# Optimization experiments

Hardware: AMD Instinct MI355X
Metric: run time of the kernel (lower is better)

## Reference

```python
import jax, jax.numpy as jnp
import numpy as np

GAMMA = 0.99
EPS = 1e-05
K = 8192   # num_embeddings
D = 256    # embed_dim
B, T = 32, 1024

def setup_inputs() -> dict:
    key = jax.random.key(0)
    k1, k2 = jax.random.split(key)
    ze = jax.random.normal(k1, (B, T, D), dtype=jnp.float32)
    embedW = jax.random.normal(k2, (K, D), dtype=jnp.float32)
    mt = jnp.zeros((K, D), dtype=jnp.float32)
    Nt = jnp.zeros((K,), dtype=jnp.float32)
    return {"ze": ze, "embedW": embedW, "mt": mt, "Nt": Nt}

def reference(ze, embedW, mt, Nt):
    b = ze.shape[0]
    ze_flat = ze.reshape(-1, ze.shape[-1])                      # [N, D]
    # squared euclidean distances: ||z||^2 - 2 z W^T + ||w||^2  -> [N, K]
    dist_mat = (jnp.sum(ze_flat * ze_flat, axis=1, keepdims=True)
                - 2.0 * ze_flat @ embedW.T
                + jnp.sum(embedW * embedW, axis=1)[None, :])
    zq_idx = jnp.argmin(dist_mat, axis=-1)                      # [N]
    zq = embedW[zq_idx]                                         # gather [N, D]
    # EMA codebook update (training mode), one-hot scatter expressed as segment sums
    nt = jax.ops.segment_sum(jnp.ones_like(zq_idx, dtype=jnp.float32), zq_idx, num_segments=K)
    Nt_new = GAMMA * Nt + (1.0 - GAMMA) * nt
    st = jax.ops.segment_sum(ze_flat, zq_idx, num_segments=K)   # one_hot.T @ ze
    mt_new = GAMMA * mt + (1.0 - GAMMA) * st
    n = jnp.sum(Nt_new)
    Nn = (Nt_new + EPS) * n / (n + K * EPS)
    embedW_new = mt_new / Nn[:, None]
    zq = zq.reshape(b, -1, zq.shape[-1])                        # [B, T, D]
    zq_idx = zq_idx.reshape(b, -1)                              # [B, T]
    commit = jnp.mean((jax.lax.stop_gradient(zq) - ze) ** 2)
    zq_st = ze + jax.lax.stop_gradient(zq - ze)                 # straight-through
    return (zq_st, commit, zq_idx, embedW_new, mt_new, Nt_new)
```

## Files before the change

### kernel.cpp

```cpp
#include <hip/hip_runtime.h>
#include <cstddef>
#include <cstdint>

#define GAMMA_F 0.99f
#define OMG_F   0.01f
#define EPS_F   1e-5f
#define KN 8192
#define DD 256
#define NN 32768

#define OFF_ZQ     0
#define OFF_COMMIT 8388608
#define OFF_IDX    8388609
#define OFF_EMB    8421377
#define OFF_MT     10518529
#define OFF_NT     12615681

#define C1 32
#define NCH1 (NN / C1)
#define NREC (NCH1 * 2)
#define C2 32
#define NCH2 (NREC / C2)

typedef _Float16 half8 __attribute__((ext_vector_type(8)));
typedef _Float16 half4 __attribute__((ext_vector_type(4)));
typedef float    f32x4 __attribute__((ext_vector_type(4)));
typedef unsigned long long u64;

__device__ __forceinline__ void gload16(const void* g, void* l) {
    __builtin_amdgcn_global_load_lds(
        (const __attribute__((address_space(1))) unsigned int*)g,
        (__attribute__((address_space(3))) unsigned int*)l, 16, 0, 0);
}

__device__ __forceinline__ u64 packdi(float dist, int n) {
    unsigned u = __float_as_uint(dist);
    u ^= (unsigned)((int)u >> 31) | 0x80000000u;
    return ((u64)u << 32) | (unsigned)n;
}

__global__ __launch_bounds__(256) void conv_hi_kernel(
    const float* __restrict__ x, _Float16* __restrict__ hi) {
    const size_t i0 = ((size_t)blockIdx.x * 256 + threadIdx.x) * 4;
    const float4 v = *(const float4*)(x + i0);
    half4 h;
    h[0] = (_Float16)v.x; h[1] = (_Float16)v.y;
    h[2] = (_Float16)v.z; h[3] = (_Float16)v.w;
    *(half4*)(hi + i0) = h;
}

__global__ __launch_bounds__(64) void convw_wsq_kernel(
    const float* __restrict__ W, _Float16* __restrict__ wh,
    float* __restrict__ wsq) {
    const int k = blockIdx.x;
    const int lane = threadIdx.x;
    const float4 v = *(const float4*)(W + (size_t)k * DD + lane * 4);
    half4 h;
    h[0] = (_Float16)v.x; h[1] = (_Float16)v.y;
    h[2] = (_Float16)v.z; h[3] = (_Float16)v.w;
    *(half4*)(wh + (size_t)k * DD + lane * 4) = h;
    float s = v.x * v.x + v.y * v.y + v.z * v.z + v.w * v.w;
#pragma unroll
    for (int off = 32; off > 0; off >>= 1) s += __shfl_down(s, off, 64);
    if (lane == 0) wsq[k] = s;
}

__global__ __launch_bounds__(256, 4) void screen_kernel(
    const _Float16* __restrict__ zh, const _Float16* __restrict__ wh,
    const float* __restrict__ wsq, u64* __restrict__ tmin2) {
    __shared__ __align__(16) _Float16 As[128 * 64];
    __shared__ __align__(16) _Float16 Bs[128 * 64];
    __shared__ __align__(16) u64 top2[128][2];

    const int tid  = threadIdx.x;
    const int wave = tid >> 6;
    const int lane = tid & 63;
    const int quad = lane >> 4;
    const int col  = lane & 15;
    const int ph = wave & 1;
    const int ch = wave >> 1;
    const int pw = ph * 64;
    const int cw = ch * 64;

    const int bm = blockIdx.x >> 6;
    const int bn = blockIdx.x & 63;
    const int m0 = bm * 128;
    const int n0 = bn * 128;

    f32x4 acc[4][4];
#pragma unroll
    for (int i = 0; i < 4; i++)
#pragma unroll
        for (int j = 0; j < 4; j++) acc[i][j] = (f32x4){0.f, 0.f, 0.f, 0.f};

    for (int c = 0; c < 4; ++c) {
        const int d0 = c * 64;
        __syncthreads();
#pragma unroll
        for (int i = 0; i < 4; ++i) {
            const int clin = (wave * 4 + i) * 64 + lane;
            const int mrow = clin >> 3;
            const int p = clin & 7;
            const int q = p ^ (mrow & 7);
            gload16(zh + (size_t)(m0 + mrow) * DD + d0 + q * 8,
                    As + (wave * 4 + i) * 512);
            gload16(wh + (size_t)(n0 + mrow) * DD + d0 + q * 8,
                    Bs + (wave * 4 + i) * 512);
        }
        __syncthreads();

#pragma unroll
        for (int kk = 0; kk < 2; ++kk) {
            half8 a[4], b[4];
#pragma unroll
            for (int t = 0; t < 4; ++t) {
                const int cr = cw + t * 16 + col;
                const int pr = pw + t * 16 + col;
                const int cc = kk * 4 + quad;
                a[t] = *(const half8*)(Bs + cr * 64 + (cc ^ (cr & 7)) * 8);
                b[t] = *(const half8*)(As + pr * 64 + (cc ^ (pr & 7)) * 8);
            }
#pragma unroll
            for (int ci = 0; ci < 4; ++ci)
#pragma unroll
                for (int pj = 0; pj < 4; ++pj)
                    acc[ci][pj] = __builtin_amdgcn_mfma_f32_16x16x32_f16(
                        a[ci], b[pj], acc[ci][pj], 0, 0, 0);
        }
    }

    float wq[4][4];
#pragma unroll
    for (int ci = 0; ci < 4; ++ci) {
        const float4 t = *(const float4*)(wsq + n0 + cw + ci * 16 + quad * 4);
        wq[ci][0] = t.x + 4096.f; wq[ci][1] = t.y + 4096.f;
        wq[ci][2] = t.z + 4096.f; wq[ci][3] = t.w + 4096.f;
    }
    const unsigned base7 = (unsigned)(cw + quad * 4);

#pragma unroll
    for (int pj = 0; pj < 4; ++pj) {
        unsigned t0 = 0xFFFFFFFFu, t1 = 0xFFFFFFFFu;
#pragma unroll
        for (int ci = 0; ci < 4; ++ci)
#pragma unroll
            for (int v = 0; v < 4; ++v) {
                const float dist = fmaf(-2.0f, acc[ci][pj][v], wq[ci][v]);
                const unsigned x = (__float_as_uint(dist) & ~127u) |
                                   (base7 + ci * 16 + v);
                const unsigned mx = t0 > x ? t0 : x;
                t0 = t0 < x ? t0 : x;
                t1 = t1 < mx ? t1 : mx;
            }
#pragma unroll
        for (int mk = 16; mk < 64; mk <<= 1) {
            const unsigned o0 = __shfl_xor(t0, mk, 64);
            const unsigned o1 = __shfl_xor(t1, mk, 64);
            const unsigned lo = t0 < o0 ? t0 : o0;
            const unsigned hi = t0 < o0 ? o0 : t0;
            const unsigned mn = t1 < o1 ? t1 : o1;
            t0 = lo;
            t1 = hi < mn ? hi : mn;
        }
        if (quad == 0)
            top2[pw + pj * 16 + col][ch] = ((u64)t1 << 32) | t0;
    }
    __syncthreads();
    if (tid < 128) {
        const u64 e0 = top2[tid][0], e1 = top2[tid][1];
        const unsigned a0 = (unsigned)e0, a1 = (unsigned)(e0 >> 32);
        const unsigned b0 = (unsigned)e1, b1 = (unsigned)(e1 >> 32);
        const unsigned t0 = a0 < b0 ? a0 : b0;
        const unsigned hi = a0 < b0 ? b0 : a0;
        const unsigned mn = a1 < b1 ? a1 : b1;
        const unsigned t1 = hi < mn ? hi : mn;
        const unsigned c1 = n0 + (t0 & 127u);
        const unsigned c2 = n0 + (t1 & 127u);
        const u64 ent = (u64)(t0 & ~127u) | ((u64)c1 << 32) | ((u64)c2 << 48);
        tmin2[(size_t)bn * NN + m0 + tid] = ent;
    }
}

__global__ __launch_bounds__(256) void compact_kernel(
    const u64* __restrict__ tmin2,
    unsigned* __restrict__ cnt, unsigned* __restrict__ slots,
    unsigned* __restrict__ hist_zero,
    const float* __restrict__ mt_in, float* __restrict__ mt_out) {
    const int tid = threadIdx.x;
    const int gid = blockIdx.x * 256 + tid;
    if (gid < KN) hist_zero[gid] = 0u;
    if (gid < KN * DD / 4) {
        const float4 m = *(const float4*)(mt_in + (size_t)gid * 4);
        float4 r;
        r.x = GAMMA_F * m.x; r.y = GAMMA_F * m.y;
        r.z = GAMMA_F * m.z; r.w = GAMMA_F * m.w;
        *(float4*)(mt_out + (size_t)gid * 4) = r;
    }

    const int lane = tid & 63;
    const int n = blockIdx.x * 4 + (tid >> 6);
    const u64 e = tmin2[(size_t)lane * NN + n];
    const float d1 = __uint_as_float((unsigned)e);
    float mn = d1;
#pragma unroll
    for (int off = 32; off > 0; off >>= 1)
        mn = fminf(mn, __shfl_xor(mn, off, 64));
    const bool q = d1 <= mn + 1.0f;
    const u64 bal = __ballot(q);
    if (q) {
        const int rank = __popcll(bal & ((1ull << lane) - 1ull));
        if (rank < 16) {
            slots[(size_t)n * 32 + 2 * rank + 0] = (unsigned)(e >> 32) & 0xffffu;
            slots[(size_t)n * 32 + 2 * rank + 1] = (unsigned)(e >> 48);
        }
    }
    if (lane == 0) {
        unsigned c = 2u * (unsigned)__popcll(bal);
        cnt[n] = c < 32u ? c : 32u;
    }
}

__global__ __launch_bounds__(256) void rescore_gather_kernel(
    const float* __restrict__ ze, const float* __restrict__ W,
    const unsigned* __restrict__ cnt, const unsigned* __restrict__ slots,
    float* __restrict__ idxf, float* __restrict__ zq_out,
    unsigned* __restrict__ hist, float* __restrict__ partials) {
    const int tid = threadIdx.x;
    const int lane = tid & 63;
    const int n = blockIdx.x * 4 + (tid >> 6);
    const float4 z = *(const float4*)(ze + (size_t)n * DD + lane * 4);
    const unsigned m = cnt[n];
    u64 best = ~0ull;
    for (unsigned j = 0; j < m; ++j) {
        const unsigned c = slots[(size_t)n * 32 + j];
        const float4 w = *(const float4*)(W + (size_t)c * DD + lane * 4);
        float dot = z.x * w.x + z.y * w.y + z.z * w.z + z.w * w.w;
        float wq  = w.x * w.x + w.y * w.y + w.z * w.z + w.w * w.w;
#pragma unroll
        for (int off = 32; off > 0; off >>= 1) {
            dot += __shfl_xor(dot, off, 64);
            wq  += __shfl_xor(wq, off, 64);
        }
        const float dist = fmaf(-2.0f, dot, wq);
        const u64 pk = packdi(dist, (int)c);
        best = best < pk ? best : pk;
    }
    const int idx = (int)(unsigned)(best & 0xFFFFFFFFull);
    if (lane == 0) {
        idxf[n] = (float)idx;
        atomicAdd(hist + idx, 1u);
    }

    const float4 w = *(const float4*)(W + (size_t)idx * DD + lane * 4);
    float4 d, o;
    d.x = w.x - z.x; d.y = w.y - z.y; d.z = w.z - z.z; d.w = w.w - z.w;
    o.x = z.x + d.x; o.y = z.y + d.y; o.z = z.z + d.z; o.w = z.w + d.w;
    *(float4*)(zq_out + (size_t)n * DD + lane * 4) = o;

    float c = d.x * d.x + d.y * d.y + d.z * d.z + d.w * d.w;
#pragma unroll
    for (int off = 32; off > 0; off >>= 1) c += __shfl_down(c, off, 64);

    __shared__ float wsum[4];
    if (lane == 0) wsum[tid >> 6] = c;
    __syncthreads();
    if (tid == 0)
        partials[blockIdx.x] = wsum[0] + wsum[1] + wsum[2] + wsum[3];
}

__global__ __launch_bounds__(256) void prefix_kernel(
    const float* __restrict__ Nt_in, float* __restrict__ ntn,
    const float* __restrict__ partials, float* __restrict__ commit_out,
    unsigned* __restrict__ offsets) {
    const int t = threadIdx.x;
    unsigned* hist = (unsigned*)ntn;
    const int base = t * 32;
    unsigned loc[32];
    unsigned sum = 0;
#pragma unroll
    for (int i = 0; i < 32; ++i) { loc[i] = hist[base + i]; sum += loc[i]; }

    __shared__ unsigned ssum[256];
    __shared__ float cred[256];
    ssum[t] = sum;
    float cp = 0.f;
    for (int i = t; i < NN / 4; i += 256) cp += partials[i];
    cred[t] = cp;
    __syncthreads();

    for (int off = 1; off < 256; off <<= 1) {
        const unsigned v = (t >= off) ? ssum[t - off] : 0u;
        __syncthreads();
        ssum[t] += v;
        __syncthreads();
    }
    unsigned run = (t > 0) ? ssum[t - 1] : 0u;

    for (int off = 128; off > 0; off >>= 1) {
        if (t < off) cred[t] += cred[t + off];
        __syncthreads();
    }
    if (t == 0) *commit_out = cred[0] * (1.0f / 8388608.0f);

#pragma unroll
    for (int i = 0; i < 32; ++i) {
        offsets[base + i] = run;
        run += loc[i];
    }
#pragma unroll
    for (int i = 0; i < 32; ++i)
        ntn[base + i] = GAMMA_F * Nt_in[base + i] + OMG_F * (float)loc[i];
}

__global__ __launch_bounds__(256) void scatter_kernel(
    const float* __restrict__ idxf, unsigned* __restrict__ offsets,
    unsigned* __restrict__ perm, unsigned* __restrict__ codes) {
    const int n = blockIdx.x * 256 + threadIdx.x;
    const int idx = (int)idxf[n];
    const unsigned pos = atomicAdd(offsets + idx, 1u);
    perm[pos] = n;
    codes[pos] = (unsigned)idx;
}

__global__ __launch_bounds__(256) void mt1_kernel(
    const float* __restrict__ ze, const float* __restrict__ mt_in,
    const unsigned* __restrict__ perm, const unsigned* __restrict__ codes,
    float* __restrict__ mt_out, unsigned* __restrict__ prec,
    float* __restrict__ pdata) {
    const int tid = threadIdx.x;
    const int lane = tid & 63;
    const int w = blockIdx.x * 4 + (tid >> 6);
    const int j0 = w * C1;

    unsigned ccur = codes[j0];
    bool first = true;
    float4 acc = {0.f, 0.f, 0.f, 0.f};

    for (int j = j0; j < j0 + C1; ++j) {
        const unsigned c = codes[j];
        if (c != ccur) {
            if (first) {
                *(float4*)(pdata + (size_t)(2 * w) * DD + lane * 4) = acc;
                if (lane == 0) prec[2 * w] = ccur;
                first = false;
            } else {
                const size_t o = (size_t)ccur * DD + lane * 4;
                const float4 m = *(const float4*)(mt_in + o);
                float4 r;
                r.x = GAMMA_F * m.x + OMG_F * acc.x;
                r.y = GAMMA_F * m.y + OMG_F * acc.y;
                r.z = GAMMA_F * m.z + OMG_F * acc.z;
                r.w = GAMMA_F * m.w + OMG_F * acc.w;
                *(float4*)(mt_out + o) = r;
            }
            acc = (float4){0.f, 0.f, 0.f, 0.f};
            ccur = c;
        }
        const unsigned p = perm[j];
        const float4 z = *(const float4*)(ze + (size_t)p * DD + lane * 4);
        acc.x += z.x; acc.y += z.y; acc.z += z.z; acc.w += z.w;
    }
    if (first) {
        *(float4*)(pdata + (size_t)(2 * w) * DD + lane * 4) = acc;
        *(float4*)(pdata + (size_t)(2 * w + 1) * DD + lane * 4) =
            (float4){0.f, 0.f, 0.f, 0.f};
        if (lane == 0) { prec[2 * w] = ccur; prec[2 * w + 1] = ccur; }
    } else {
        *(float4*)(pdata + (size_t)(2 * w + 1) * DD + lane * 4) = acc;
        if (lane == 0) prec[2 * w + 1] = ccur;
    }
}

__global__ __launch_bounds__(256) void mt2_kernel(
    const float* __restrict__ mt_in, const unsigned* __restrict__ prec,
    const float* __restrict__ pdata, float* __restrict__ mt_out) {
    const int tid = threadIdx.x;
    const int lane = tid & 63;
    const int w = blockIdx.x * 4 + (tid >> 6);
    const int r0 = w * C2;

    unsigned ccur = prec[r0];
    bool first = true;
    float4 acc = {0.f, 0.f, 0.f, 0.f};

    for (int r = r0; r < r0 + C2; ++r) {
        const unsigned c = prec[r];
        if (c != ccur) {
            if (first) {
                float* mp = mt_out + (size_t)ccur * DD + lane * 4;
                atomicAdd(mp + 0, OMG_F * acc.x);
                atomicAdd(mp + 1, OMG_F * acc.y);
                atomicAdd(mp + 2, OMG_F * acc.z);
                atomicAdd(mp + 3, OMG_F * acc.w);
                first = false;
            } else {
                const size_t o = (size_t)ccur * DD + lane * 4;
                const float4 m = *(const float4*)(mt_in + o);
                float4 rr;
                rr.x = GAMMA_F * m.x + OMG_F * acc.x;
                rr.y = GAMMA_F * m.y + OMG_F * acc.y;
                rr.z = GAMMA_F * m.z + OMG_F * acc.z;
                rr.w = GAMMA_F * m.w + OMG_F * acc.w;
                *(float4*)(mt_out + o) = rr;
            }
            acc = (float4){0.f, 0.f, 0.f, 0.f};
            ccur = c;
        }
        const float4 v = *(const float4*)(pdata + (size_t)r * DD + lane * 4);
        acc.x += v.x; acc.y += v.y; acc.z += v.z; acc.w += v.w;
    }
    float* mp = mt_out + (size_t)ccur * DD + lane * 4;
    atomicAdd(mp + 0, OMG_F * acc.x);
    atomicAdd(mp + 1, OMG_F * acc.y);
    atomicAdd(mp + 2, OMG_F * acc.z);
    atomicAdd(mp + 3, OMG_F * acc.w);
}

__global__ __launch_bounds__(256) void final_kernel(
    const float* __restrict__ nt_new, const float* __restrict__ mt_new,
    float* __restrict__ emb_out) {
    __shared__ float red[256];
    float s = 0.0f;
    for (int i = threadIdx.x; i < KN; i += 256) s += nt_new[i];
    red[threadIdx.x] = s;
    __syncthreads();
    for (int off = 128; off > 0; off >>= 1) {
        if (threadIdx.x < off) red[threadIdx.x] += red[threadIdx.x + off];
        __syncthreads();
    }
    const float n = red[0];

    const size_t i0 = ((size_t)blockIdx.x * 256 + threadIdx.x) * 4;
    const int k = (int)(i0 >> 8);

    const float4 mt = *(const float4*)(mt_new + i0);
    const float Nn = (nt_new[k] + EPS_F) * n / (n + (float)KN * EPS_F);
    float4 e;
    e.x = mt.x / Nn;
    e.y = mt.y / Nn;
    e.z = mt.z / Nn;
    e.w = mt.w / Nn;
    *(float4*)(emb_out + i0) = e;
}

extern "C" void kernel_launch(void* const* d_in, const int* in_sizes, int n_in,
                              void* d_out, int out_size, void* d_ws, size_t ws_size,
                              hipStream_t stream) {
    const float* ze = (const float*)d_in[0];
    const float* W  = (const float*)d_in[1];
    const float* mt = (const float*)d_in[2];
    const float* Nt = (const float*)d_in[3];

    float* out    = (float*)d_out;
    float* zq_out = out + OFF_ZQ;
    float* commit = out + OFF_COMMIT;
    float* idxf   = out + OFF_IDX;
    float* emb    = out + OFF_EMB;
    float* mtn    = out + OFF_MT;
    float* ntn    = out + OFF_NT;

    _Float16* zh = (_Float16*)zq_out;
    u64* tmin2 =
        (u64*)(zq_out + (size_t)NN * DD / 2);
    _Float16* wh = (_Float16*)(mtn + 3);
    float* wsqbuf = idxf + 3;
    unsigned* cnt      = (unsigned*)emb;
    unsigned* slots    = cnt + NN;
    float*    partials = (float*)(slots + (size_t)NN * 32);
    unsigned* offsets  = (unsigned*)partials + NN / 4;
    unsigned* perm     = offsets + KN;
    unsigned* codes    = perm + NN;
    unsigned* prec     = codes + NN;
    float*    pdata    = (float*)(prec + NREC);
    unsigned* hist     = (unsigned*)ntn;

    conv_hi_kernel<<<(NN * DD / 4) / 256, 256, 0, stream>>>(ze, zh);
    convw_wsq_kernel<<<KN, 64, 0, stream>>>(W, wh, wsqbuf);

    screen_kernel<<<(NN / 128) * (KN / 128), 256, 0, stream>>>(
        zh, wh, wsqbuf, tmin2);

    compact_kernel<<<NN / 4, 256, 0, stream>>>(tmin2, cnt, slots, hist,
                                               mt, mtn);

    rescore_gather_kernel<<<NN / 4, 256, 0, stream>>>(
        ze, W, cnt, slots, idxf, zq_out, hist, partials);

    prefix_kernel<<<1, 256, 0, stream>>>(Nt, ntn, partials, commit, offsets);

    scatter_kernel<<<NN / 256, 256, 0, stream>>>(idxf, offsets, perm, codes);

    mt1_kernel<<<NCH1 / 4, 256, 0, stream>>>(ze, mt, perm, codes, mtn,
                                             prec, pdata);

    mt2_kernel<<<NCH2 / 4, 256, 0, stream>>>(mt, prec, pdata, mtn);

    final_kernel<<<(KN * DD / 4) / 256, 256, 0, stream>>>(ntn, mtn, emb);
}
```

Baseline: 381.8 us.

## Enlarge screen GEMM tile to 256x256 with double-buffered LDS staging

The screening GEMM now runs 512-thread blocks over 256x256 tiles instead of 128x128, and each wave computes a 64x128 sub-tile. K-chunks are double-buffered in LDS so the next chunk's global loads are issued before computing the current one, with one barrier per chunk. The intent is to cut global/L2 traffic per FLOP and overlap loads with MFMA work. In exchange it uses 128 KB of LDS per block and 128 accumulator registers per thread, which lowers occupancy and risks register pressure. The per-row top-2 output keeps the same 128-column record layout as before.

```diff
diff --git a/kernel.cpp b/kernel.cpp
--- a/kernel.cpp
+++ b/kernel.cpp
@@ -65,81 +65,89 @@
     if (lane == 0) wsq[k] = s;
 }
 
-__global__ __launch_bounds__(256, 4) void screen_kernel(
+__global__ __launch_bounds__(512, 2) void screen_kernel(
     const _Float16* __restrict__ zh, const _Float16* __restrict__ wh,
     const float* __restrict__ wsq, u64* __restrict__ tmin2) {
-    __shared__ __align__(16) _Float16 As[128 * 64];
-    __shared__ __align__(16) _Float16 Bs[128 * 64];
-    __shared__ __align__(16) u64 top2[128][2];
+    __shared__ __align__(16) _Float16 As[2][256 * 64];
+    __shared__ __align__(16) _Float16 Bs[2][256 * 64];
+    __shared__ __align__(16) u64 top2[256][4];
 
     const int tid  = threadIdx.x;
     const int wave = tid >> 6;
     const int lane = tid & 63;
     const int quad = lane >> 4;
     const int col  = lane & 15;
-    const int ph = wave & 1;
-    const int ch = wave >> 1;
-    const int pw = ph * 64;
-    const int cw = ch * 64;
-
-    const int bm = blockIdx.x >> 6;
-    const int bn = blockIdx.x & 63;
-    const int m0 = bm * 128;
-    const int n0 = bn * 128;
-
-    f32x4 acc[4][4];
+    const int ph = wave >> 2;
+    const int cq = wave & 3;
+
+    const int bm = blockIdx.x >> 5;
+    const int bn = blockIdx.x & 31;
+    const int m0 = bm * 256;
+    const int n0 = bn * 256;
+
+    f32x4 acc[4][8];
 #pragma unroll
     for (int i = 0; i < 4; i++)
 #pragma unroll
-        for (int j = 0; j < 4; j++) acc[i][j] = (f32x4){0.f, 0.f, 0.f, 0.f};
+        for (int j = 0; j < 8; j++) acc[i][j] = (f32x4){0.f, 0.f, 0.f, 0.f};
+
+    auto stage = [&](int b, int c) {
+        const int d0 = c * 64;
+#pragma unroll
+        for (int t = 0; t < 4; ++t) {
+            const int clin = (wave * 4 + t) * 64 + lane;
+            const int mrow = clin >> 3;
+            const int q = (clin & 7) ^ (mrow & 7);
+            gload16(zh + (size_t)(m0 + mrow) * DD + d0 + q * 8,
+                    &As[b][(wave * 4 + t) * 512]);
+            gload16(wh + (size_t)(n0 + mrow) * DD + d0 + q * 8,
+                    &Bs[b][(wave * 4 + t) * 512]);
+        }
+    };
+
+    stage(0, 0);
+    __syncthreads();
 
     for (int c = 0; c < 4; ++c) {
-        const int d0 = c * 64;
-        __syncthreads();
-#pragma unroll
-        for (int i = 0; i < 4; ++i) {
-            const int clin = (wave * 4 + i) * 64 + lane;
-            const int mrow = clin >> 3;
-            const int p = clin & 7;
-            const int q = p ^ (mrow & 7);
-            gload16(zh + (size_t)(m0 + mrow) * DD + d0 + q * 8,
-                    As + (wave * 4 + i) * 512);
-            gload16(wh + (size_t)(n0 + mrow) * DD + d0 + q * 8,
-                    Bs + (wave * 4 + i) * 512);
-        }
-        __syncthreads();
-
+        if (c < 3) stage((c + 1) & 1, c + 1);
+        const _Float16* Ab = As[c & 1];
+        const _Float16* Bb = Bs[c & 1];
 #pragma unroll
         for (int kk = 0; kk < 2; ++kk) {
-            half8 a[4], b[4];
+            half8 a[4], b[8];
+            const int cc = kk * 4 + quad;
 #pragma unroll
             for (int t = 0; t < 4; ++t) {
-                const int cr = cw + t * 16 + col;
-                const int pr = pw + t * 16 + col;
-                const int cc = kk * 4 + quad;
-                a[t] = *(const half8*)(Bs + cr * 64 + (cc ^ (cr & 7)) * 8);
-                b[t] = *(const half8*)(As + pr * 64 + (cc ^ (pr & 7)) * 8);
+                const int cr = cq * 64 + t * 16 + col;
+                a[t] = *(const half8*)(Bb + cr * 64 + (cc ^ (cr & 7)) * 8);
             }
 #pragma unroll
+            for (int t = 0; t < 8; ++t) {
+                const int pr = ph * 128 + t * 16 + col;
+                b[t] = *(const half8*)(Ab + pr * 64 + (cc ^ (pr & 7)) * 8);
+            }
+#pragma unroll
             for (int ci = 0; ci < 4; ++ci)
 #pragma unroll
-                for (int pj = 0; pj < 4; ++pj)
+                for (int pj = 0; pj < 8; ++pj)
                     acc[ci][pj] = __builtin_amdgcn_mfma_f32_16x16x32_f16(
                         a[ci], b[pj], acc[ci][pj], 0, 0, 0);
         }
+        __syncthreads();
     }
 
     float wq[4][4];
 #pragma unroll
     for (int ci = 0; ci < 4; ++ci) {
-        const float4 t = *(const float4*)(wsq + n0 + cw + ci * 16 + quad * 4);
+        const float4 t =
+            *(const float4*)(wsq + n0 + cq * 64 + ci * 16 + quad * 4);
         wq[ci][0] = t.x + 4096.f; wq[ci][1] = t.y + 4096.f;
         wq[ci][2] = t.z + 4096.f; wq[ci][3] = t.w + 4096.f;
     }
-    const unsigned base7 = (unsigned)(cw + quad * 4);
-
-#pragma unroll
-    for (int pj = 0; pj < 4; ++pj) {
+    const unsigned base7 = (unsigned)((cq & 1) * 64 + quad * 4);
+
+#pragma unroll
+    for (int pj = 0; pj < 8; ++pj) {
         unsigned t0 = 0xFFFFFFFFu, t1 = 0xFFFFFFFFu;
 #pragma unroll
         for (int ci = 0; ci < 4; ++ci)
@@ -163,21 +171,23 @@
             t1 = hi < mn ? hi : mn;
         }
         if (quad == 0)
-            top2[pw + pj * 16 + col][ch] = ((u64)t1 << 32) | t0;
+            top2[ph * 128 + pj * 16 + col][cq] = ((u64)t1 << 32) | t0;
     }
     __syncthreads();
-    if (tid < 128) {
-        const u64 e0 = top2[tid][0], e1 = top2[tid][1];
+    {
+        const int p = tid & 255;
+        const int h = tid >> 8;
+        const u64 e0 = top2[p][2 * h], e1 = top2[p][2 * h + 1];
         const unsigned a0 = (unsigned)e0, a1 = (unsigned)(e0 >> 32);
         const unsigned b0 = (unsigned)e1, b1 = (unsigned)(e1 >> 32);
         const unsigned t0 = a0 < b0 ? a0 : b0;
         const unsigned hi = a0 < b0 ? b0 : a0;
         const unsigned mn = a1 < b1 ? a1 : b1;
         const unsigned t1 = hi < mn ? hi : mn;
-        const unsigned c1 = n0 + (t0 & 127u);
-        const unsigned c2 = n0 + (t1 & 127u);
+        const unsigned c1 = n0 + h * 128 + (t0 & 127u);
+        const unsigned c2 = n0 + h * 128 + (t1 & 127u);
         const u64 ent = (u64)(t0 & ~127u) | ((u64)c1 << 32) | ((u64)c2 << 48);
-        tmin2[(size_t)bn * NN + m0 + tid] = ent;
+        tmin2[(size_t)(bn * 2 + h) * NN + m0 + p] = ent;
     }
 }
 
@@ -477,7 +487,7 @@
     conv_hi_kernel<<<(NN * DD / 4) / 256, 256, 0, stream>>>(ze, zh);
     convw_wsq_kernel<<<KN, 64, 0, stream>>>(W, wh, wsqbuf);
 
-    screen_kernel<<<(NN / 128) * (KN / 128), 256, 0, stream>>>(
+    screen_kernel<<<(NN / 256) * (KN / 256), 512, 0, stream>>>(
         zh, wh, wsqbuf, tmin2);
 
     compact_kernel<<<NN / 4, 256, 0, stream>>>(tmin2, cnt, slots, hist,
```

Result: slower. 391.1 us (+2.4%).

## Fuse prep, compact+rescore kernels and hoist codebook-count reduction into prefix

Applied to the files above, without the earlier changes.

Merges the two conversion kernels into one prep kernel that also zeroes the histogram, and fuses compaction with rescore so candidate slots stay in shared memory instead of a global slots/cnt buffer. The screen output is split into separate lo/hi 32-bit arrays, the mt gamma-scaling moves into the scatter kernel, and the Nt sum is computed once in prefix rather than by every final_kernel block. This removes launches, global round-trips and redundant reductions. The trade-off is a reshuffled workspace layout with aliased output buffers, which is fragile.

```diff
diff --git a/kernel.cpp b/kernel.cpp
--- a/kernel.cpp
+++ b/kernel.cpp
@@ -39,35 +39,42 @@
     return ((u64)u << 32) | (unsigned)n;
 }
 
-__global__ __launch_bounds__(256) void conv_hi_kernel(
-    const float* __restrict__ x, _Float16* __restrict__ hi) {
-    const size_t i0 = ((size_t)blockIdx.x * 256 + threadIdx.x) * 4;
-    const float4 v = *(const float4*)(x + i0);
-    half4 h;
-    h[0] = (_Float16)v.x; h[1] = (_Float16)v.y;
-    h[2] = (_Float16)v.z; h[3] = (_Float16)v.w;
-    *(half4*)(hi + i0) = h;
-}
-
-__global__ __launch_bounds__(64) void convw_wsq_kernel(
-    const float* __restrict__ W, _Float16* __restrict__ wh,
-    float* __restrict__ wsq) {
-    const int k = blockIdx.x;
-    const int lane = threadIdx.x;
-    const float4 v = *(const float4*)(W + (size_t)k * DD + lane * 4);
-    half4 h;
-    h[0] = (_Float16)v.x; h[1] = (_Float16)v.y;
-    h[2] = (_Float16)v.z; h[3] = (_Float16)v.w;
-    *(half4*)(wh + (size_t)k * DD + lane * 4) = h;
-    float s = v.x * v.x + v.y * v.y + v.z * v.z + v.w * v.w;
-#pragma unroll
-    for (int off = 32; off > 0; off >>= 1) s += __shfl_down(s, off, 64);
-    if (lane == 0) wsq[k] = s;
+__global__ __launch_bounds__(256) void prep_kernel(
+    const float* __restrict__ ze, const float* __restrict__ W,
+    _Float16* __restrict__ zh, _Float16* __restrict__ wh,
+    float* __restrict__ wsq, unsigned* __restrict__ hist_zero) {
+    const int tid = threadIdx.x;
+    const size_t gid = (size_t)blockIdx.x * 256 + tid;
+
+    {
+        const size_t i0 = gid * 4;
+        const float4 v = *(const float4*)(ze + i0);
+        half4 h;
+        h[0] = (_Float16)v.x; h[1] = (_Float16)v.y;
+        h[2] = (_Float16)v.z; h[3] = (_Float16)v.w;
+        *(half4*)(zh + i0) = h;
+    }
+    if (gid < KN) hist_zero[gid] = 0u;
+
+    if (blockIdx.x < KN / 4) {
+        const int k = blockIdx.x * 4 + (tid >> 6);
+        const int lane = tid & 63;
+        const float4 v = *(const float4*)(W + (size_t)k * DD + lane * 4);
+        half4 h;
+        h[0] = (_Float16)v.x; h[1] = (_Float16)v.y;
+        h[2] = (_Float16)v.z; h[3] = (_Float16)v.w;
+        *(half4*)(wh + (size_t)k * DD + lane * 4) = h;
+        float s = v.x * v.x + v.y * v.y + v.z * v.z + v.w * v.w;
+#pragma unroll
+        for (int off = 32; off > 0; off >>= 1) s += __shfl_down(s, off, 64);
+        if (lane == 0) wsq[k] = s;
+    }
 }
 
 __global__ __launch_bounds__(256, 4) void screen_kernel(
     const _Float16* __restrict__ zh, const _Float16* __restrict__ wh,
-    const float* __restrict__ wsq, u64* __restrict__ tmin2) {
+    const float* __restrict__ wsq,
+    unsigned* __restrict__ tlo, unsigned* __restrict__ thi) {
     __shared__ __align__(16) _Float16 As[128 * 64];
     __shared__ __align__(16) _Float16 Bs[128 * 64];
     __shared__ __align__(16) u64 top2[128][2];
@@ -177,30 +184,26 @@
         const unsigned c1 = n0 + (t0 & 127u);
         const unsigned c2 = n0 + (t1 & 127u);
         const u64 ent = (u64)(t0 & ~127u) | ((u64)c1 << 32) | ((u64)c2 << 48);
-        tmin2[(size_t)bn * NN + m0 + tid] = ent;
-    }
-}
-
-__global__ __launch_bounds__(256) void compact_kernel(
-    const u64* __restrict__ tmin2,
-    unsigned* __restrict__ cnt, unsigned* __restrict__ slots,
-    unsigned* __restrict__ hist_zero,
-    const float* __restrict__ mt_in, float* __restrict__ mt_out) {
+        tlo[(size_t)bn * NN + m0 + tid] = (unsigned)ent;
+        thi[(size_t)bn * NN + m0 + tid] = (unsigned)(ent >> 32);
+    }
+}
+
+__global__ __launch_bounds__(256) void select_kernel(
+    const unsigned* __restrict__ tlo, const unsigned* __restrict__ thi,
+    const float* __restrict__ ze, const float* __restrict__ W,
+    float* __restrict__ idxf, float* __restrict__ zq_out,
+    unsigned* __restrict__ hist, float* __restrict__ partials) {
+    __shared__ unsigned sl[4][32];
+    __shared__ float wsum[4];
     const int tid = threadIdx.x;
-    const int gid = blockIdx.x * 256 + tid;
-    if (gid < KN) hist_zero[gid] = 0u;
-    if (gid < KN * DD / 4) {
-        const float4 m = *(const float4*)(mt_in + (size_t)gid * 4);
-        float4 r;
-        r.x = GAMMA_F * m.x; r.y = GAMMA_F * m.y;
-        r.z = GAMMA_F * m.z; r.w = GAMMA_F * m.w;
-        *(float4*)(mt_out + (size_t)gid * 4) = r;
-    }
-
     const int lane = tid & 63;
-    const int n = blockIdx.x * 4 + (tid >> 6);
-    const u64 e = tmin2[(size_t)lane * NN + n];
-    const float d1 = __uint_as_float((unsigned)e);
+    const int w = tid >> 6;
+
+    const int n = blockIdx.x * 4 + w;
+    const unsigned elo = tlo[(size_t)lane * NN + n];
+    const unsigned ehi = thi[(size_t)lane * NN + n];
+    const float d1 = __uint_as_float(elo);
     float mn = d1;
 #pragma unroll
     for (int off = 32; off > 0; off >>= 1)
@@ -210,32 +213,21 @@
     if (q) {
         const int rank = __popcll(bal & ((1ull << lane) - 1ull));
         if (rank < 16) {
-            slots[(size_t)n * 32 + 2 * rank + 0] = (unsigned)(e >> 32) & 0xffffu;
-            slots[(size_t)n * 32 + 2 * rank + 1] = (unsigned)(e >> 48);
-        }
-    }
-    if (lane == 0) {
-        unsigned c = 2u * (unsigned)__popcll(bal);
-        cnt[n] = c < 32u ? c : 32u;
-    }
-}
-
-__global__ __launch_bounds__(256) void rescore_gather_kernel(
-    const float* __restrict__ ze, const float* __restrict__ W,
-    const unsigned* __restrict__ cnt, const unsigned* __restrict__ slots,
-    float* __restrict__ idxf, float* __restrict__ zq_out,
-    unsigned* __restrict__ hist, float* __restrict__ partials) {
-    const int tid = threadIdx.x;
-    const int lane = tid & 63;
-    const int n = blockIdx.x * 4 + (tid >> 6);
+            sl[w][2 * rank + 0] = ehi & 0xffffu;
+            sl[w][2 * rank + 1] = ehi >> 16;
+        }
+    }
+    unsigned m = 2u * (unsigned)__popcll(bal);
+    m = m < 32u ? m : 32u;
+    __syncthreads();
+
     const float4 z = *(const float4*)(ze + (size_t)n * DD + lane * 4);
-    const unsigned m = cnt[n];
     u64 best = ~0ull;
     for (unsigned j = 0; j < m; ++j) {
-        const unsigned c = slots[(size_t)n * 32 + j];
-        const float4 w = *(const float4*)(W + (size_t)c * DD + lane * 4);
-        float dot = z.x * w.x + z.y * w.y + z.z * w.z + z.w * w.w;
-        float wq  = w.x * w.x + w.y * w.y + w.z * w.z + w.w * w.w;
+        const unsigned c = sl[w][j];
+        const float4 ww = *(const float4*)(W + (size_t)c * DD + lane * 4);
+        float dot = z.x * ww.x + z.y * ww.y + z.z * ww.z + z.w * ww.w;
+        float wq  = ww.x * ww.x + ww.y * ww.y + ww.z * ww.z + ww.w * ww.w;
 #pragma unroll
         for (int off = 32; off > 0; off >>= 1) {
             dot += __shfl_xor(dot, off, 64);
@@ -251,9 +243,9 @@
         atomicAdd(hist + idx, 1u);
     }
 
-    const float4 w = *(const float4*)(W + (size_t)idx * DD + lane * 4);
+    const float4 ww = *(const float4*)(W + (size_t)idx * DD + lane * 4);
     float4 d, o;
-    d.x = w.x - z.x; d.y = w.y - z.y; d.z = w.z - z.z; d.w = w.w - z.w;
+    d.x = ww.x - z.x; d.y = ww.y - z.y; d.z = ww.z - z.z; d.w = ww.w - z.w;
     o.x = z.x + d.x; o.y = z.y + d.y; o.z = z.z + d.z; o.w = z.w + d.w;
     *(float4*)(zq_out + (size_t)n * DD + lane * 4) = o;
 
@@ -261,17 +253,16 @@
 #pragma unroll
     for (int off = 32; off > 0; off >>= 1) c += __shfl_down(c, off, 64);
 
-    __shared__ float wsum[4];
-    if (lane == 0) wsum[tid >> 6] = c;
+    if (lane == 0) wsum[w] = c;
     __syncthreads();
     if (tid == 0)
-        partials[blockIdx.x] = wsum[0] + wsum[1] + wsum[2] + wsum[3];
+        partials[4 * blockIdx.x] = wsum[0] + wsum[1] + wsum[2] + wsum[3];
 }
 
 __global__ __launch_bounds__(256) void prefix_kernel(
     const float* __restrict__ Nt_in, float* __restrict__ ntn,
     const float* __restrict__ partials, float* __restrict__ commit_out,
-    unsigned* __restrict__ offsets) {
+    unsigned* __restrict__ offsets, float* __restrict__ nws) {
     const int t = threadIdx.x;
     unsigned* hist = (unsigned*)ntn;
     const int base = t * 32;
@@ -282,9 +273,10 @@
 
     __shared__ unsigned ssum[256];
     __shared__ float cred[256];
+    __shared__ float fred[256];
     ssum[t] = sum;
     float cp = 0.f;
-    for (int i = t; i < NN / 4; i += 256) cp += partials[i];
+    for (int i = t; i < NN / 4; i += 256) cp += partials[4 * i];
     cred[t] = cp;
     __syncthreads();
 
@@ -307,19 +299,40 @@
         offsets[base + i] = run;
         run += loc[i];
     }
-#pragma unroll
-    for (int i = 0; i < 32; ++i)
-        ntn[base + i] = GAMMA_F * Nt_in[base + i] + OMG_F * (float)loc[i];
+    float fs = 0.f;
+#pragma unroll
+    for (int i = 0; i < 32; ++i) {
+        const float v = GAMMA_F * Nt_in[base + i] + OMG_F * (float)loc[i];
+        ntn[base + i] = v;
+        fs += v;
+    }
+    fred[t] = fs;
+    __syncthreads();
+    for (int off = 128; off > 0; off >>= 1) {
+        if (t < off) fred[t] += fred[t + off];
+        __syncthreads();
+    }
+    if (t == 0) nws[0] = fred[0];
 }
 
 __global__ __launch_bounds__(256) void scatter_kernel(
     const float* __restrict__ idxf, unsigned* __restrict__ offsets,
-    unsigned* __restrict__ perm, unsigned* __restrict__ codes) {
-    const int n = blockIdx.x * 256 + threadIdx.x;
-    const int idx = (int)idxf[n];
-    const unsigned pos = atomicAdd(offsets + idx, 1u);
-    perm[pos] = n;
-    codes[pos] = (unsigned)idx;
+    unsigned* __restrict__ perm, unsigned* __restrict__ codes,
+    const float* __restrict__ mt_in, float* __restrict__ mt_out) {
+    const size_t gid = (size_t)blockIdx.x * 256 + threadIdx.x;
+    {
+        const float4 m = *(const float4*)(mt_in + gid * 4);
+        float4 r;
+        r.x = GAMMA_F * m.x; r.y = GAMMA_F * m.y;
+        r.z = GAMMA_F * m.z; r.w = GAMMA_F * m.w;
+        *(float4*)(mt_out + gid * 4) = r;
+    }
+    if (gid < NN) {
+        const int idx = (int)idxf[gid];
+        const unsigned pos = atomicAdd(offsets + idx, 1u);
+        perm[pos] = (unsigned)gid;
+        codes[pos] = (unsigned)idx;
+    }
 }
 
 __global__ __launch_bounds__(256) void mt1_kernel(
@@ -418,18 +431,8 @@
 
 __global__ __launch_bounds__(256) void final_kernel(
     const float* __restrict__ nt_new, const float* __restrict__ mt_new,
-    float* __restrict__ emb_out) {
-    __shared__ float red[256];
-    float s = 0.0f;
-    for (int i = threadIdx.x; i < KN; i += 256) s += nt_new[i];
-    red[threadIdx.x] = s;
-    __syncthreads();
-    for (int off = 128; off > 0; off >>= 1) {
-        if (threadIdx.x < off) red[threadIdx.x] += red[threadIdx.x + off];
-        __syncthreads();
-    }
-    const float n = red[0];
-
+    const float* __restrict__ nws, float* __restrict__ emb_out) {
+    const float n = nws[0];
     const size_t i0 = ((size_t)blockIdx.x * 256 + threadIdx.x) * 4;
     const int k = (int)(i0 >> 8);
 
@@ -460,40 +463,38 @@
     float* ntn    = out + OFF_NT;
 
     _Float16* zh = (_Float16*)zq_out;
-    u64* tmin2 =
-        (u64*)(zq_out + (size_t)NN * DD / 2);
-    _Float16* wh = (_Float16*)(mtn + 3);
-    float* wsqbuf = idxf + 3;
-    unsigned* cnt      = (unsigned*)emb;
-    unsigned* slots    = cnt + NN;
-    float*    partials = (float*)(slots + (size_t)NN * 32);
-    unsigned* offsets  = (unsigned*)partials + NN / 4;
-    unsigned* perm     = offsets + KN;
-    unsigned* codes    = perm + NN;
-    unsigned* prec     = codes + NN;
-    float*    pdata    = (float*)(prec + NREC);
-    unsigned* hist     = (unsigned*)ntn;
-
-    conv_hi_kernel<<<(NN * DD / 4) / 256, 256, 0, stream>>>(ze, zh);
-    convw_wsq_kernel<<<KN, 64, 0, stream>>>(W, wh, wsqbuf);
+    _Float16* wh = (_Float16*)(zq_out + (size_t)NN * DD / 2);
+    float* wsqbuf = zq_out + (size_t)NN * DD / 2 + (size_t)KN * DD / 2;
+    unsigned* tlo = (unsigned*)emb;
+    unsigned* thi = tlo + (size_t)64 * NN;
+    float* partials = (float*)tlo;
+    unsigned* offsets = tlo;
+    unsigned* perm    = tlo + 8192;
+    unsigned* codes   = tlo + 40960;
+    unsigned* prec    = tlo + 73728;
+    float*    pdata   = (float*)tlo + 75779;
+    unsigned* hist    = (unsigned*)ntn;
+    float*    nws     = (float*)d_ws;
+
+    prep_kernel<<<(NN * DD / 4) / 256, 256, 0, stream>>>(
+        ze, W, zh, wh, wsqbuf, hist);
 
     screen_kernel<<<(NN / 128) * (KN / 128), 256, 0, stream>>>(
-        zh, wh, wsqbuf, tmin2);
-
-    compact_kernel<<<NN / 4, 256, 0, stream>>>(tmin2, cnt, slots, hist,
-                                               mt, mtn);
-
-    rescore_gather_kernel<<<NN / 4, 256, 0, stream>>>(
-        ze, W, cnt, slots, idxf, zq_out, hist, partials);
-
-    prefix_kernel<<<1, 256, 0, stream>>>(Nt, ntn, partials, commit, offsets);
-
-    scatter_kernel<<<NN / 256, 256, 0, stream>>>(idxf, offsets, perm, codes);
+        zh, wh, wsqbuf, tlo, thi);
+
+    select_kernel<<<NN / 4, 256, 0, stream>>>(
+        tlo, thi, ze, W, idxf, zq_out, hist, partials);
+
+    prefix_kernel<<<1, 256, 0, stream>>>(Nt, ntn, partials, commit,
+                                         offsets, nws);
+
+    scatter_kernel<<<(KN * DD / 4) / 256, 256, 0, stream>>>(
+        idxf, offsets, perm, codes, mt, mtn);
 
     mt1_kernel<<<NCH1 / 4, 256, 0, stream>>>(ze, mt, perm, codes, mtn,
                                              prec, pdata);
 
     mt2_kernel<<<NCH2 / 4, 256, 0, stream>>>(mt, prec, pdata, mtn);
 
-    final_kernel<<<(KN * DD / 4) / 256, 256, 0, stream>>>(ntn, mtn, emb);
-}
+    final_kernel<<<(KN * DD / 4) / 256, 256, 0, stream>>>(ntn, mtn, nws, emb);
+}
```

After: 362.7 us. 5.0% less time.
